# Optimization experiments

Measured on AMD Instinct MI355X. Metric: run time of the kernel, lower is better.

Reference implementation:

```python
import jax, jax.numpy as jnp
import numpy as np

N_STEPS = 5
STATE_DIM = 512
ANN_DIM = 256
N_NODES = 2048
N_EDGE_TYPES = 4


def setup_inputs() -> dict:
    key = jax.random.key(0)
    ks = jax.random.split(key, 12)
    D, E, N = STATE_DIM, N_EDGE_TYPES, N_NODES
    s = 0.02
    adjacency = (jax.random.uniform(ks[0], (N, N * 2 * E)) < 0.015).astype(jnp.float32)
    annotations = jax.random.normal(ks[1], (N, ANN_DIM), dtype=jnp.float32)
    W_prop = jax.random.normal(ks[2], (2 * E, D, D), dtype=jnp.float32) * s
    b_prop = jnp.zeros((2 * E, D), dtype=jnp.float32)
    Wz = jax.random.normal(ks[3], (D, D), dtype=jnp.float32) * s
    Uz = jax.random.normal(ks[4], (D, D), dtype=jnp.float32) * s
    bz = jnp.zeros((D,), dtype=jnp.float32)
    Wr = jax.random.normal(ks[5], (D, D), dtype=jnp.float32) * s
    Ur = jax.random.normal(ks[6], (D, D), dtype=jnp.float32) * s
    br = jnp.zeros((D,), dtype=jnp.float32)
    Wh = jax.random.normal(ks[7], (D, D), dtype=jnp.float32) * s
    Uh = jax.random.normal(ks[8], (D, D), dtype=jnp.float32) * s
    bh = jnp.zeros((D,), dtype=jnp.float32)
    return dict(adjacency=adjacency, annotations=annotations, W_prop=W_prop, b_prop=b_prop,
                Wz=Wz, Uz=Uz, bz=bz, Wr=Wr, Ur=Ur, br=br, Wh=Wh, Uh=Uh, bh=bh)


def reference(adjacency, annotations, W_prop, b_prop, Wz, Uz, bz, Wr, Ur, br, Wh, Uh, bh):
    N = annotations.shape[0]
    D = W_prop.shape[-1]
    # pad annotations into first columns of state (input1[:, :ann_dim] = annotations)
    h = jnp.zeros((N, D), dtype=annotations.dtype).at[:, :annotations.shape[1]].set(annotations)
    for _ in range(N_STEPS):
        # per-edge-type linear transforms: edge_type_list [2E, N, D]
        t = jnp.einsum('nd,edf->enf', h, W_prop) + b_prop[:, None, :]
        # adjacency aggregation: A is [N, N*2E] with per-edge-type column blocks
        a = adjacency @ t.reshape(-1, D)  # [N, D]
        # GRU node update (UpdateNet)
        z = jax.nn.sigmoid(a @ Wz + h @ Uz + bz)
        r = jax.nn.sigmoid(a @ Wr + h @ Ur + br)
        h_tilde = jnp.tanh(a @ Wh + (r * h) @ Uh + bh)
        h = (1.0 - z) * h + z * h_tilde
    return h
```

## Files before the change

kernel.cpp:

```cpp
#include <hip/hip_runtime.h>

typedef __attribute__((ext_vector_type(8))) short short8;
typedef __attribute__((ext_vector_type(4))) float floatx4;

#define NSTEPS 5
#define DD 512
#define ANN 256
#define NNODE 2048
#define NEDGE 8
#define NCOLS (NNODE * NEDGE)
#define MAXE 96
#define KP (NEDGE * DD)


typedef __attribute__((address_space(3))) unsigned lds_u32;
typedef const __attribute__((address_space(1))) unsigned g_u32;
__device__ __forceinline__ void gload16(const short* g, short* l) {
    __builtin_amdgcn_global_load_lds((g_u32*)g, (lds_u32*)l, 16, 0, 0);
}

__device__ inline float bf2f(unsigned short s) {
    unsigned u = ((unsigned)s) << 16;
    float f; __builtin_memcpy(&f, &u, 4);
    return f;
}
__device__ inline unsigned short f2bf(float f) {
    unsigned u; __builtin_memcpy(&u, &f, 4);
    u += 0x7fffu + ((u >> 16) & 1u);
    return (unsigned short)(u >> 16);
}
__device__ inline void split2(float x, unsigned short& hi, unsigned short& lo) {
    hi = f2bf(x);
    lo = f2bf(x - bf2f(hi));
}
__device__ inline void fo_write(short* __restrict__ Fhi, short* __restrict__ Flo,
                                int row, int col, float v) {
    unsigned short hs, ls;
    split2(v, hs, ls);
    size_t a = ((size_t)(row >> 4) * 64 + (col >> 3)) * 128 + ((row & 15) << 3) + (col & 7);
    Fhi[a] = (short)hs;
    Flo[a] = (short)ls;
}
__device__ inline void fo_write2(short* __restrict__ Fhi, short* __restrict__ Flo,
                                 int row, int c, float v0, float v1) {
    unsigned short h0, l0, h1, l1;
    split2(v0, h0, l0);
    split2(v1, h1, l1);
    size_t a = ((size_t)(row >> 4) * 64 + (c >> 3)) * 128 + ((row & 15) << 3) + (c & 7);
    *(unsigned*)(Fhi + a) = (unsigned)h0 | ((unsigned)h1 << 16);
    *(unsigned*)(Flo + a) = (unsigned)l0 | ((unsigned)l1 << 16);
}

__global__ __launch_bounds__(256) void k_init(const float* __restrict__ ann,
                                              float* __restrict__ h,
                                              short* __restrict__ HBhi,
                                              short* __restrict__ HBlo,
                                              int* __restrict__ cnt2) {
    int n = blockIdx.x, t = threadIdx.x;
    int c = 2 * t;
    float v0 = 0.f, v1 = 0.f;
    if (c < ANN) {
        v0 = ann[(size_t)n * ANN + c];
        v1 = ann[(size_t)n * ANN + c + 1];
    }
    h[(size_t)n * DD + c]     = v0;
    h[(size_t)n * DD + c + 1] = v1;
    fo_write2(HBhi, HBlo, n, c, v0, v1);
    if (t < NEDGE) cnt2[n * NEDGE + t] = 0;
}

__global__ __launch_bounds__(256) void k_build(const float* __restrict__ adj,
                                               int* __restrict__ cnt2,
                                               unsigned short* __restrict__ idx) {
    int n = blockIdx.x;
    const float* row = adj + (size_t)n * NCOLS;
    for (int j8 = threadIdx.x; j8 < NCOLS / 8; j8 += 256) {
        floatx4 a = *(const floatx4*)(row + j8 * 8);
        floatx4 b = *(const floatx4*)(row + j8 * 8 + 4);
        unsigned nz = 0;
        #pragma unroll
        for (int i = 0; i < 4; i++) {
            if (a[i] != 0.f) nz |= 1u << i;
            if (b[i] != 0.f) nz |= 1u << (4 + i);
        }
        while (nz) {
            int i = __builtin_ctz(nz);
            nz &= nz - 1;
            int j = j8 * 8 + i;
            int e = j >> 11;
            int m = j & (NNODE - 1);
            int p = atomicAdd(&cnt2[n * NEDGE + e], 1);
            if (p < MAXE) idx[((size_t)n * NEDGE + e) * MAXE + p] = (unsigned short)m;
        }
    }
}

__global__ __launch_bounds__(256) void k_transP(const float* __restrict__ W,
                                                short* __restrict__ Fhi,
                                                short* __restrict__ Flo, int K) {
    __shared__ float st[32][33];
    int tx = threadIdx.x & 31, ty = threadIdx.x >> 5;
    int k0 = blockIdx.x * 32, n0 = blockIdx.y * 32;
    #pragma unroll
    for (int i = 0; i < 4; i++)
        st[ty + i * 8][tx] = W[(size_t)(k0 + ty + i * 8) * DD + n0 + tx];
    __syncthreads();
    #pragma unroll
    for (int i = 0; i < 4; i++) {
        int n = n0 + ty + i * 8, k = k0 + tx;
        float v = st[tx][ty + i * 8];
        unsigned short hs, ls;
        split2(v, hs, ls);
        size_t a = ((size_t)(n >> 4) * (K >> 3) + (k >> 3)) * 128 + ((n & 15) << 3) + (k & 7);
        Fhi[a] = (short)hs;
        Flo[a] = (short)ls;
    }
}

__global__ __launch_bounds__(256) void k_transG(const float* __restrict__ s00,
                                                const float* __restrict__ s10,
                                                const float* __restrict__ s01,
                                                const float* __restrict__ s11,
                                                short* __restrict__ Fhi,
                                                short* __restrict__ Flo) {
    __shared__ float st[32][33];
    const int K = 2 * DD;
    int tx = threadIdx.x & 31, ty = threadIdx.x >> 5;
    int k0 = blockIdx.x * 32, n0 = blockIdx.y * 32;
    const float* sk0 = (n0 < DD) ? s00 : s01;
    const float* sk1 = (n0 < DD) ? s10 : s11;
    #pragma unroll
    for (int i = 0; i < 4; i++) {
        int k = k0 + ty + i * 8;
        const float* s = (k < DD) ? sk0 : sk1;
        st[ty + i * 8][tx] = s[(size_t)(k & (DD - 1)) * DD + ((n0 + tx) & (DD - 1))];
    }
    __syncthreads();
    #pragma unroll
    for (int i = 0; i < 4; i++) {
        int n = n0 + ty + i * 8, k = k0 + tx;
        float v = st[tx][ty + i * 8];
        unsigned short hs, ls;
        split2(v, hs, ls);
        size_t a = ((size_t)(n >> 4) * (K >> 3) + (k >> 3)) * 128 + ((n & 15) << 3) + (k & 7);
        Fhi[a] = (short)hs;
        Flo[a] = (short)ls;
    }
}

__global__ __launch_bounds__(256) void k_gather_all(const float* __restrict__ h,
                                                    const int* __restrict__ cnt2,
                                                    const unsigned short* __restrict__ idx,
                                                    const float* __restrict__ bp,
                                                    short* __restrict__ Gbhi,
                                                    short* __restrict__ Gblo,
                                                    float* __restrict__ abuf) {
    __shared__ unsigned short sidx[NEDGE * MAXE];
    __shared__ int scnt[NEDGE];
    int n = blockIdx.x, t = threadIdx.x;

    if (t < NEDGE) scnt[t] = cnt2[n * NEDGE + t];
    for (int j = t; j < NEDGE * MAXE / 2; j += 256)
        ((unsigned*)sidx)[j] = ((const unsigned*)(idx + (size_t)n * NEDGE * MAXE))[j];
    __syncthreads();

    const int th = t & 127;
    const int eg = t >> 7;
    size_t wbase = ((size_t)(n >> 4) * 512) * 128 + ((n & 15) << 3) + ((th & 1) << 2);

    #pragma unroll 1
    for (int ee = 0; ee < 4; ee++) {
        int e = eg * 4 + ee;
        int raw = scnt[e];
        int m = raw > MAXE ? MAXE : raw;
        const unsigned short* row = &sidx[e * MAXE];
        floatx4 a0 = (floatx4){0.f, 0.f, 0.f, 0.f};
        floatx4 a1 = (floatx4){0.f, 0.f, 0.f, 0.f};
        int i = 0;
        for (; i + 16 <= m; i += 16) {
            #pragma unroll
            for (int j = 0; j < 8; j++) {
                a0 += *(const floatx4*)(h + (size_t)row[i + j] * DD + 4 * th);
                a1 += *(const floatx4*)(h + (size_t)row[i + 8 + j] * DD + 4 * th);
            }
        }
        if (i + 8 <= m) {
            #pragma unroll
            for (int j = 0; j < 8; j++)
                a0 += *(const floatx4*)(h + (size_t)row[i + j] * DD + 4 * th);
            i += 8;
        }
        if (i + 4 <= m) {
            #pragma unroll
            for (int j = 0; j < 4; j++)
                a1 += *(const floatx4*)(h + (size_t)row[i + j] * DD + 4 * th);
            i += 4;
        }
        for (; i < m; i++)
            a0 += *(const floatx4*)(h + (size_t)row[i] * DD + 4 * th);
        floatx4 a = a0 + a1;

        unsigned short hs[4], ls[4];
        #pragma unroll
        for (int j = 0; j < 4; j++) split2(a[j], hs[j], ls[j]);
        unsigned long long hp = (unsigned long long)hs[0] | ((unsigned long long)hs[1] << 16)
                              | ((unsigned long long)hs[2] << 32) | ((unsigned long long)hs[3] << 48);
        unsigned long long lp = (unsigned long long)ls[0] | ((unsigned long long)ls[1] << 16)
                              | ((unsigned long long)ls[2] << 32) | ((unsigned long long)ls[3] << 48);
        size_t addr = wbase + (size_t)(e * 64 + (th >> 1)) * 128;
        __builtin_nontemporal_store(hp, (unsigned long long*)(Gbhi + addr));
        __builtin_nontemporal_store(lp, (unsigned long long*)(Gblo + addr));
    }

    if (eg == 0) {
        floatx4 s = (floatx4){0.f, 0.f, 0.f, 0.f};
        #pragma unroll
        for (int e = 0; e < NEDGE; e++)
            s += (float)scnt[e] * *(const floatx4*)(bp + e * DD + 4 * th);
        __builtin_nontemporal_store(s, (floatx4*)(abuf + (size_t)n * DD + 4 * th));
    }
}

template<int MODE>
__global__ __launch_bounds__(256, 4) void k_gemm8(
    const short* __restrict__ A0hi, const short* __restrict__ A0lo,
    const short* __restrict__ A1hi, const short* __restrict__ A1lo,
    const short* __restrict__ Bhi,  const short* __restrict__ Blo,
    const float* __restrict__ bias0, const float* __restrict__ bias1,
    float* __restrict__ zbuf,
    float* __restrict__ h,
    short* __restrict__ Ohi, short* __restrict__ Olo,
    float* __restrict__ P0, float* __restrict__ P1) {

    __shared__ short S[24][512];

    const int tid = threadIdx.x;
    const int lane = tid & 63;
    const int wave = tid >> 6;
    const int wm = wave >> 1;
    const int wn = wave & 1;
    const int quad = lane >> 4;
    const int l16 = lane & 15;

    const int pbid = blockIdx.x;
    const int x = pbid & 7;
    const int j = pbid >> 3;
    const int mband = x * 4 + (j & 3);
    int kh, bx;
    if (MODE == 1) { kh = 0; bx = j >> 2; }
    else           { kh = (j >> 2) & 1; bx = j >> 3; }
    const int blockM = mband * 64;
    const int blockN = bx * 32;
    const int mt0 = blockM >> 4, nt0 = blockN >> 4;
    const int KCB = (MODE == 0) ? 512 : 128;
    const int bko = (MODE == 0) ? kh * 256 : (MODE == 2 ? kh * 64 : 0);
    const int Kloc = (MODE == 0) ? 2048 : (MODE == 1 ? 1024 : 512);

    const short* Ahi_s = (MODE == 2 && kh) ? A1hi : A0hi;
    const short* Alo_s = (MODE == 2 && kh) ? A1lo : A0lo;

    floatx4 acc[2];
    acc[0] = (floatx4){0.f, 0.f, 0.f, 0.f};
    acc[1] = (floatx4){0.f, 0.f, 0.f, 0.f};

    auto gaddr = [&](int k0, int s) -> const short* {
        if (s < 16) {
            int pl = s >> 3, u = s & 7;
            int mt = u >> 1, ks = u & 1;
            const short* base;
            int kc, stride;
            if (MODE == 0) {
                base = pl ? A0lo : A0hi;
                kc = kh * 256 + (k0 >> 3) + ks * 4;
                stride = 512;
            } else if (MODE == 1) {
                int seg = k0 >> 9;
                base = seg ? (pl ? A1lo : A1hi) : (pl ? A0lo : A0hi);
                kc = ((k0 & 511) >> 3) + ks * 4;
                stride = 64;
            } else {
                base = pl ? Alo_s : Ahi_s;
                kc = (k0 >> 3) + ks * 4;
                stride = 64;
            }
            return base + ((size_t)(mt0 + mt) * stride + kc) * 128;
        } else {
            int u = s - 16, pl = u >> 2, ks = (u >> 1) & 1, nt = u & 1;
            const short* base = pl ? Blo : Bhi;
            return base + ((size_t)(nt0 + nt) * KCB + bko + (k0 >> 3) + ks * 4) * 128;
        }
    };

    for (int k0 = 0; k0 < Kloc; k0 += 64) {
        #pragma unroll
        for (int jj = 0; jj < 6; jj++) {
            int s = jj * 4 + wave;
            gload16(gaddr(k0, s) + lane * 8, &S[s][lane * 8]);
        }
        __syncthreads();

        #pragma unroll
        for (int ks = 0; ks < 2; ks++) {
            short8 ah[2], al[2], bh, bl;
            #pragma unroll
            for (int mi = 0; mi < 2; mi++) {
                ah[mi] = *(const short8*)&S[(wm * 2 + mi) * 2 + ks][lane * 8];
                al[mi] = *(const short8*)&S[8 + (wm * 2 + mi) * 2 + ks][lane * 8];
            }
            bh = *(const short8*)&S[16 + ks * 2 + wn][lane * 8];
            bl = *(const short8*)&S[20 + ks * 2 + wn][lane * 8];
            #pragma unroll
            for (int mi = 0; mi < 2; mi++) {
                acc[mi] = __builtin_amdgcn_mfma_f32_16x16x32_bf16(ah[mi], bh, acc[mi], 0, 0, 0);
                acc[mi] = __builtin_amdgcn_mfma_f32_16x16x32_bf16(ah[mi], bl, acc[mi], 0, 0, 0);
                acc[mi] = __builtin_amdgcn_mfma_f32_16x16x32_bf16(al[mi], bh, acc[mi], 0, 0, 0);
            }
        }
        __syncthreads();
    }

    float* P = kh ? P1 : P0;
    #pragma unroll
    for (int mi = 0; mi < 2; mi++) {
        int gcol = blockN + wn * 16 + l16;
        #pragma unroll
        for (int r = 0; r < 4; r++) {
            int grow = blockM + wm * 32 + mi * 16 + quad * 4 + r;
            float v = acc[mi][r];
            if (MODE == 0 || MODE == 2) {
                P[(size_t)grow * DD + gcol] = v;
            } else {
                if (gcol < DD) {
                    size_t o = (size_t)grow * DD + gcol;
                    zbuf[o] = 1.f / (1.f + __expf(-(v + bias0[gcol])));
                } else {
                    int c = gcol - DD;
                    size_t o = (size_t)grow * DD + c;
                    float rr = 1.f / (1.f + __expf(-(v + bias1[c])));
                    fo_write(Ohi, Olo, grow, c, rr * h[o]);
                }
            }
        }
    }
}

__global__ __launch_bounds__(256) void k_combP(const float* __restrict__ P0,
                                               const float* __restrict__ P1,
                                               const float* __restrict__ abuf,
                                               short* __restrict__ Gahi,
                                               short* __restrict__ Galo) {
    int n = blockIdx.x, t = threadIdx.x;
    size_t o = (size_t)n * DD + 2 * t;
    float v0 = P0[o] + P1[o] + abuf[o];
    float v1 = P0[o + 1] + P1[o + 1] + abuf[o + 1];
    fo_write2(Gahi, Galo, n, 2 * t, v0, v1);
}

__global__ __launch_bounds__(256) void k_combF(const float* __restrict__ P0,
                                               const float* __restrict__ P1,
                                               const float* __restrict__ bh,
                                               const float* __restrict__ zbuf,
                                               float* __restrict__ h,
                                               short* __restrict__ HBhi,
                                               short* __restrict__ HBlo,
                                               float* __restrict__ outF) {
    int n = blockIdx.x, t = threadIdx.x;
    int c = 2 * t;
    size_t o = (size_t)n * DD + c;
    float hn0, hn1;
    {
        float v = P0[o] + P1[o] + bh[c];
        hn0 = (1.f - zbuf[o]) * h[o] + zbuf[o] * tanhf(v);
    }
    {
        float v = P0[o + 1] + P1[o + 1] + bh[c + 1];
        hn1 = (1.f - zbuf[o + 1]) * h[o + 1] + zbuf[o + 1] * tanhf(v);
    }
    h[o] = hn0;
    h[o + 1] = hn1;
    fo_write2(HBhi, HBlo, n, c, hn0, hn1);
    outF[o] = hn0;
    outF[o + 1] = hn1;
}

extern "C" void kernel_launch(void* const* d_in, const int* in_sizes, int n_in,
                              void* d_out, int out_size, void* d_ws, size_t ws_size,
                              hipStream_t stream) {
    const float* adj = (const float*)d_in[0];
    const float* ann = (const float*)d_in[1];
    const float* Wp  = (const float*)d_in[2];
    const float* bp  = (const float*)d_in[3];
    const float* Wz  = (const float*)d_in[4];
    const float* Uz  = (const float*)d_in[5];
    const float* bz  = (const float*)d_in[6];
    const float* Wr  = (const float*)d_in[7];
    const float* Ur  = (const float*)d_in[8];
    const float* br  = (const float*)d_in[9];
    const float* Wh  = (const float*)d_in[10];
    const float* Uh  = (const float*)d_in[11];
    const float* bh  = (const float*)d_in[12];

    char* p = (char*)d_ws;
    float* h     = (float*)p; p += (size_t)NNODE * DD * 4;
    float* abuf  = (float*)p; p += (size_t)NNODE * DD * 4;
    float* P0    = (float*)p; p += (size_t)NNODE * DD * 4;
    float* P1    = (float*)p; p += (size_t)NNODE * DD * 4;
    short* Gbhi  = (short*)p; p += (size_t)NNODE * KP * 2;
    short* Gblo  = (short*)p; p += (size_t)NNODE * KP * 2;
    short* Gahi  = (short*)p; p += (size_t)NNODE * DD * 2;
    short* Galo  = (short*)p; p += (size_t)NNODE * DD * 2;
    short* HBhi  = (short*)p; p += (size_t)NNODE * DD * 2;
    short* HBlo  = (short*)p; p += (size_t)NNODE * DD * 2;
    short* RHhi  = (short*)p; p += (size_t)NNODE * DD * 2;
    short* RHlo  = (short*)p; p += (size_t)NNODE * DD * 2;
    short* WpThi = (short*)p; p += (size_t)DD * KP * 2;
    short* WpTlo = (short*)p; p += (size_t)DD * KP * 2;
    short* ZRhi  = (short*)p; p += (size_t)(2 * DD) * (2 * DD) * 2;
    short* ZRlo  = (short*)p; p += (size_t)(2 * DD) * (2 * DD) * 2;
    short* HThi  = (short*)p; p += (size_t)DD * (2 * DD) * 2;
    short* HTlo  = (short*)p; p += (size_t)DD * (2 * DD) * 2;
    unsigned short* idx = (unsigned short*)p;
    p += (size_t)NNODE * NEDGE * MAXE * 2;
    int* cnt2 = (int*)p; p += (size_t)NNODE * NEDGE * 4;

    float* outF = (float*)d_out;

    k_init<<<NNODE, 256, 0, stream>>>(ann, h, HBhi, HBlo, cnt2);
    k_build<<<NNODE, 256, 0, stream>>>(adj, cnt2, idx);
    k_transP<<<dim3(KP / 32, DD / 32), 256, 0, stream>>>(Wp, WpThi, WpTlo, KP);
    k_transG<<<dim3(32, 32), 256, 0, stream>>>(Wz, Uz, Wr, Ur, ZRhi, ZRlo);
    k_transG<<<dim3(32, 16), 256, 0, stream>>>(Wh, Uh, Wh, Uh, HThi, HTlo);

    for (int s = 0; s < NSTEPS; s++) {
        k_gather_all<<<NNODE, 256, 0, stream>>>(h, cnt2, idx, bp, Gbhi, Gblo, abuf);
        k_gemm8<0><<<1024, 256, 0, stream>>>(Gbhi, Gblo, nullptr, nullptr,
                                             WpThi, WpTlo, nullptr, nullptr,
                                             nullptr, nullptr, nullptr, nullptr, P0, P1);
        k_combP<<<NNODE, 256, 0, stream>>>(P0, P1, abuf, Gahi, Galo);
        k_gemm8<1><<<1024, 256, 0, stream>>>(Gahi, Galo, HBhi, HBlo,
                                             ZRhi, ZRlo, bz, br,
                                             abuf, h, RHhi, RHlo, nullptr, nullptr);
        k_gemm8<2><<<1024, 256, 0, stream>>>(Gahi, Galo, RHhi, RHlo,
                                             HThi, HTlo, nullptr, nullptr,
                                             nullptr, nullptr, nullptr, nullptr, P0, P1);
        k_combF<<<NNODE, 256, 0, stream>>>(P0, P1, bh, abuf, h, HBhi, HBlo, outF);
    }
}
```

Before: 1.054 ms.

## Use 64x64 tiles with 4-way split-K for propagation GEMM and batch gather loads

```diff
diff --git a/kernel.cpp b/kernel.cpp
--- a/kernel.cpp
+++ b/kernel.cpp
@@ -148,13 +148,13 @@
     }
 }
 
-__global__ __launch_bounds__(256) void k_gather_all(const float* __restrict__ h,
-                                                    const int* __restrict__ cnt2,
-                                                    const unsigned short* __restrict__ idx,
-                                                    const float* __restrict__ bp,
-                                                    short* __restrict__ Gbhi,
-                                                    short* __restrict__ Gblo,
-                                                    float* __restrict__ abuf) {
+__global__ __launch_bounds__(256, 4) void k_gather_all(const float* __restrict__ h,
+                                                       const int* __restrict__ cnt2,
+                                                       const unsigned short* __restrict__ idx,
+                                                       const float* __restrict__ bp,
+                                                       short* __restrict__ Gbhi,
+                                                       short* __restrict__ Gblo,
+                                                       float* __restrict__ abuf) {
     __shared__ unsigned short sidx[NEDGE * MAXE];
     __shared__ int scnt[NEDGE];
     int n = blockIdx.x, t = threadIdx.x;
@@ -174,31 +174,39 @@
         int raw = scnt[e];
         int m = raw > MAXE ? MAXE : raw;
         const unsigned short* row = &sidx[e * MAXE];
-        floatx4 a0 = (floatx4){0.f, 0.f, 0.f, 0.f};
-        floatx4 a1 = (floatx4){0.f, 0.f, 0.f, 0.f};
+        floatx4 a = (floatx4){0.f, 0.f, 0.f, 0.f};
         int i = 0;
         for (; i + 16 <= m; i += 16) {
-            #pragma unroll
-            for (int j = 0; j < 8; j++) {
-                a0 += *(const floatx4*)(h + (size_t)row[i + j] * DD + 4 * th);
-                a1 += *(const floatx4*)(h + (size_t)row[i + 8 + j] * DD + 4 * th);
-            }
+            floatx4 v[16];
+            #pragma unroll
+            for (int j = 0; j < 16; j++)
+                v[j] = *(const floatx4*)(h + (size_t)row[i + j] * DD + 4 * th);
+            #pragma unroll
+            for (int j = 0; j < 16; j++)
+                a += v[j];
         }
         if (i + 8 <= m) {
+            floatx4 v[8];
             #pragma unroll
             for (int j = 0; j < 8; j++)
-                a0 += *(const floatx4*)(h + (size_t)row[i + j] * DD + 4 * th);
+                v[j] = *(const floatx4*)(h + (size_t)row[i + j] * DD + 4 * th);
+            #pragma unroll
+            for (int j = 0; j < 8; j++)
+                a += v[j];
             i += 8;
         }
         if (i + 4 <= m) {
+            floatx4 v[4];
             #pragma unroll
             for (int j = 0; j < 4; j++)
-                a1 += *(const floatx4*)(h + (size_t)row[i + j] * DD + 4 * th);
+                v[j] = *(const floatx4*)(h + (size_t)row[i + j] * DD + 4 * th);
+            #pragma unroll
+            for (int j = 0; j < 4; j++)
+                a += v[j];
             i += 4;
         }
         for (; i < m; i++)
-            a0 += *(const floatx4*)(h + (size_t)row[i] * DD + 4 * th);
-        floatx4 a = a0 + a1;
+            a += *(const floatx4*)(h + (size_t)row[i] * DD + 4 * th);
 
         unsigned short hs[4], ls[4];
         #pragma unroll
@@ -219,6 +227,99 @@
             s += (float)scnt[e] * *(const floatx4*)(bp + e * DD + 4 * th);
         __builtin_nontemporal_store(s, (floatx4*)(abuf + (size_t)n * DD + 4 * th));
     }
+}
+
+__global__ __launch_bounds__(256, 4) void k_gemmP(
+    const short* __restrict__ Ahi, const short* __restrict__ Alo,
+    const short* __restrict__ Bhi, const short* __restrict__ Blo,
+    float* __restrict__ P0, float* __restrict__ P1,
+    float* __restrict__ P2, float* __restrict__ P3) {
+
+    __shared__ short S[32][512];
+
+    const int tid = threadIdx.x;
+    const int lane = tid & 63;
+    const int wave = tid >> 6;
+    const int wm = wave >> 1;
+    const int wn = wave & 1;
+    const int quad = lane >> 4;
+    const int l16 = lane & 15;
+
+    const int pbid = blockIdx.x;
+    const int x = pbid & 7;
+    const int j = pbid >> 3;
+    const int mband = x * 4 + (j & 3);
+    const int kq = (j >> 2) & 3;
+    const int bx = j >> 4;
+    const int blockM = mband * 64;
+    const int blockN = bx * 64;
+    const int mt0 = blockM >> 4, nt0 = blockN >> 4;
+    const int kco = kq * 128;
+
+    floatx4 acc[2][2];
+    #pragma unroll
+    for (int mi = 0; mi < 2; mi++)
+        #pragma unroll
+        for (int ni = 0; ni < 2; ni++)
+            acc[mi][ni] = (floatx4){0.f, 0.f, 0.f, 0.f};
+
+    auto gaddr = [&](int k0, int s) -> const short* {
+        if (s < 16) {
+            int pl = s >> 3, u = s & 7, mt = u >> 1, ks = u & 1;
+            const short* base = pl ? Alo : Ahi;
+            return base + ((size_t)(mt0 + mt) * 512 + kco + (k0 >> 3) + ks * 4) * 128;
+        } else {
+            int u = s - 16, pl = u >> 3, v2 = u & 7, nt = v2 >> 1, ks = v2 & 1;
+            const short* base = pl ? Blo : Bhi;
+            return base + ((size_t)(nt0 + nt) * 512 + kco + (k0 >> 3) + ks * 4) * 128;
+        }
+    };
+
+    for (int k0 = 0; k0 < 1024; k0 += 64) {
+        #pragma unroll
+        for (int jj = 0; jj < 8; jj++) {
+            int s = wave * 8 + jj;
+            gload16(gaddr(k0, s) + lane * 8, &S[s][lane * 8]);
+        }
+        __syncthreads();
+
+        #pragma unroll
+        for (int ks = 0; ks < 2; ks++) {
+            short8 ah[2], al[2], bh[2], bl[2];
+            #pragma unroll
+            for (int mi = 0; mi < 2; mi++) {
+                ah[mi] = *(const short8*)&S[(wm * 2 + mi) * 2 + ks][lane * 8];
+                al[mi] = *(const short8*)&S[8 + (wm * 2 + mi) * 2 + ks][lane * 8];
+            }
+            #pragma unroll
+            for (int ni = 0; ni < 2; ni++) {
+                bh[ni] = *(const short8*)&S[16 + (wn * 2 + ni) * 2 + ks][lane * 8];
+                bl[ni] = *(const short8*)&S[24 + (wn * 2 + ni) * 2 + ks][lane * 8];
+            }
+            #pragma unroll
+            for (int mi = 0; mi < 2; mi++)
+                #pragma unroll
+                for (int ni = 0; ni < 2; ni++) {
+                    acc[mi][ni] = __builtin_amdgcn_mfma_f32_16x16x32_bf16(ah[mi], bh[ni], acc[mi][ni], 0, 0, 0);
+                    acc[mi][ni] = __builtin_amdgcn_mfma_f32_16x16x32_bf16(ah[mi], bl[ni], acc[mi][ni], 0, 0, 0);
+                    acc[mi][ni] = __builtin_amdgcn_mfma_f32_16x16x32_bf16(al[mi], bh[ni], acc[mi][ni], 0, 0, 0);
+                }
+        }
+        __syncthreads();
+    }
+
+    float* P = (kq == 0) ? P0 : (kq == 1) ? P1 : (kq == 2) ? P2 : P3;
+    #pragma unroll
+    for (int mi = 0; mi < 2; mi++)
+        #pragma unroll
+        for (int ni = 0; ni < 2; ni++) {
+            int gcol = blockN + wn * 32 + ni * 16 + l16;
+            #pragma unroll
+            for (int r = 0; r < 4; r++) {
+                int grow = blockM + wm * 32 + mi * 16 + quad * 4 + r;
+                P[(size_t)grow * DD + gcol] = acc[mi][ni][r];
+            }
+        }
 }
 
 template<int MODE>
@@ -252,9 +353,9 @@
     const int blockM = mband * 64;
     const int blockN = bx * 32;
     const int mt0 = blockM >> 4, nt0 = blockN >> 4;
-    const int KCB = (MODE == 0) ? 512 : 128;
-    const int bko = (MODE == 0) ? kh * 256 : (MODE == 2 ? kh * 64 : 0);
-    const int Kloc = (MODE == 0) ? 2048 : (MODE == 1 ? 1024 : 512);
+    const int KCB = 128;
+    const int bko = (MODE == 2) ? kh * 64 : 0;
+    const int Kloc = (MODE == 1) ? 1024 : 512;
 
     const short* Ahi_s = (MODE == 2 && kh) ? A1hi : A0hi;
     const short* Alo_s = (MODE == 2 && kh) ? A1lo : A0lo;
@@ -265,25 +366,18 @@
 
     auto gaddr = [&](int k0, int s) -> const short* {
         if (s < 16) {
-            int pl = s >> 3, u = s & 7;
-            int mt = u >> 1, ks = u & 1;
+            int pl = s >> 3, u = s & 7, mt = u >> 1, ks = u & 1;
             const short* base;
-            int kc, stride;
-            if (MODE == 0) {
-                base = pl ? A0lo : A0hi;
-                kc = kh * 256 + (k0 >> 3) + ks * 4;
-                stride = 512;
-            } else if (MODE == 1) {
+            int kc;
+            if (MODE == 1) {
                 int seg = k0 >> 9;
                 base = seg ? (pl ? A1lo : A1hi) : (pl ? A0lo : A0hi);
                 kc = ((k0 & 511) >> 3) + ks * 4;
-                stride = 64;
             } else {
                 base = pl ? Alo_s : Ahi_s;
                 kc = (k0 >> 3) + ks * 4;
-                stride = 64;
-            }
-            return base + ((size_t)(mt0 + mt) * stride + kc) * 128;
+            }
+            return base + ((size_t)(mt0 + mt) * 64 + kc) * 128;
         } else {
             int u = s - 16, pl = u >> 2, ks = (u >> 1) & 1, nt = u & 1;
             const short* base = pl ? Blo : Bhi;
@@ -327,9 +421,7 @@
         for (int r = 0; r < 4; r++) {
             int grow = blockM + wm * 32 + mi * 16 + quad * 4 + r;
             float v = acc[mi][r];
-            if (MODE == 0 || MODE == 2) {
-                P[(size_t)grow * DD + gcol] = v;
-            } else {
+            if (MODE == 1) {
                 if (gcol < DD) {
                     size_t o = (size_t)grow * DD + gcol;
                     zbuf[o] = 1.f / (1.f + __expf(-(v + bias0[gcol])));
@@ -339,20 +431,24 @@
                     float rr = 1.f / (1.f + __expf(-(v + bias1[c])));
                     fo_write(Ohi, Olo, grow, c, rr * h[o]);
                 }
-            }
-        }
-    }
-}
-
-__global__ __launch_bounds__(256) void k_combP(const float* __restrict__ P0,
-                                               const float* __restrict__ P1,
-                                               const float* __restrict__ abuf,
-                                               short* __restrict__ Gahi,
-                                               short* __restrict__ Galo) {
+            } else {
+                P[(size_t)grow * DD + gcol] = v;
+            }
+        }
+    }
+}
+
+__global__ __launch_bounds__(256) void k_combP4(const float* __restrict__ P0,
+                                                const float* __restrict__ P1,
+                                                const float* __restrict__ P2,
+                                                const float* __restrict__ P3,
+                                                const float* __restrict__ abuf,
+                                                short* __restrict__ Gahi,
+                                                short* __restrict__ Galo) {
     int n = blockIdx.x, t = threadIdx.x;
     size_t o = (size_t)n * DD + 2 * t;
-    float v0 = P0[o] + P1[o] + abuf[o];
-    float v1 = P0[o + 1] + P1[o + 1] + abuf[o + 1];
+    float v0 = P0[o] + P1[o] + P2[o] + P3[o] + abuf[o];
+    float v1 = P0[o + 1] + P1[o + 1] + P2[o + 1] + P3[o + 1] + abuf[o + 1];
     fo_write2(Gahi, Galo, n, 2 * t, v0, v1);
 }
 
@@ -405,6 +501,8 @@
     float* abuf  = (float*)p; p += (size_t)NNODE * DD * 4;
     float* P0    = (float*)p; p += (size_t)NNODE * DD * 4;
     float* P1    = (float*)p; p += (size_t)NNODE * DD * 4;
+    float* P2    = (float*)p; p += (size_t)NNODE * DD * 4;
+    float* P3    = (float*)p; p += (size_t)NNODE * DD * 4;
     short* Gbhi  = (short*)p; p += (size_t)NNODE * KP * 2;
     short* Gblo  = (short*)p; p += (size_t)NNODE * KP * 2;
     short* Gahi  = (short*)p; p += (size_t)NNODE * DD * 2;
@@ -433,10 +531,8 @@
 
     for (int s = 0; s < NSTEPS; s++) {
         k_gather_all<<<NNODE, 256, 0, stream>>>(h, cnt2, idx, bp, Gbhi, Gblo, abuf);
-        k_gemm8<0><<<1024, 256, 0, stream>>>(Gbhi, Gblo, nullptr, nullptr,
-                                             WpThi, WpTlo, nullptr, nullptr,
-                                             nullptr, nullptr, nullptr, nullptr, P0, P1);
-        k_combP<<<NNODE, 256, 0, stream>>>(P0, P1, abuf, Gahi, Galo);
+        k_gemmP<<<1024, 256, 0, stream>>>(Gbhi, Gblo, WpThi, WpTlo, P0, P1, P2, P3);
+        k_combP4<<<NNODE, 256, 0, stream>>>(P0, P1, P2, P3, abuf, Gahi, Galo);
         k_gemm8<1><<<1024, 256, 0, stream>>>(Gahi, Galo, HBhi, HBlo,
                                              ZRhi, ZRlo, bz, br,
                                              abuf, h, RHhi, RHlo, nullptr, nullptr);
```

Measured after the change: 1.325 ms. +25.7%, slower.
